# Performance work log

Measured on AMD Instinct MI355X. Metric: run time of the kernel, lower is better.

The kernel has to match this reference:

```python
import jax, jax.numpy as jnp
import numpy as np

D_MODEL = 1024
NUM_HEADS = 16
D_K = D_MODEL // NUM_HEADS
SCALE = float(np.sqrt(D_K))


def setup_inputs() -> dict:
    key = jax.random.key(0)
    ks = jax.random.split(key, 6)
    x = jax.random.normal(ks[0], (2, 2048, D_MODEL), dtype=jnp.float32)
    s = 1.0 / np.sqrt(D_MODEL)
    w_q = jax.random.uniform(ks[1], (D_MODEL, D_MODEL), jnp.float32, -s, s)
    w_k = jax.random.uniform(ks[2], (D_MODEL, D_MODEL), jnp.float32, -s, s)
    w_v = jax.random.uniform(ks[3], (D_MODEL, D_MODEL), jnp.float32, -s, s)
    w_o = jax.random.uniform(ks[4], (D_MODEL, D_MODEL), jnp.float32, -s, s)
    b_o = jax.random.uniform(ks[5], (D_MODEL,), jnp.float32, -s, s)
    return {"x": x, "w_q": w_q, "w_k": w_k, "w_v": w_v, "w_o": w_o, "b_o": b_o}


def reference(x, w_q, w_k, w_v, w_o, b_o):
    B, S, _ = x.shape
    # project and split heads: [B, H, S, d_k]
    def heads(w):
        return (x @ w.T).reshape(B, S, NUM_HEADS, D_K).transpose(0, 2, 1, 3)
    Q, K, V = heads(w_q), heads(w_k), heads(w_v)
    scores = jnp.einsum("bhqd,bhkd->bhqk", Q, K) / SCALE  # [B,H,S,S]
    attn = jax.nn.softmax(scores, axis=-1)
    context = jnp.einsum("bhqk,bhkd->bhqd", attn, V)
    context = context.transpose(0, 2, 1, 3).reshape(B, S, D_MODEL)
    return context @ w_o.T + b_o
```

## Files before the change

### kernel.cpp

```cpp
#include <hip/hip_runtime.h>

typedef unsigned short u16t;
typedef short bf16x8 __attribute__((ext_vector_type(8)));
typedef short bf16x4 __attribute__((ext_vector_type(4)));
typedef float f32x4 __attribute__((ext_vector_type(4)));

#define NHEADS 16
#define SEQ 2048
#define DMODEL 1024
#define HEAD_ELEMS (SEQ * 64)
#define LSTR 72
#define QSTR 40
#define MATE ((size_t)2 * SEQ * DMODEL)
#define CSC 0.1803368801f
#define MB 4.0f

__device__ __forceinline__ u16t f2bf(float f) {
  union { float f; unsigned u; } v; v.f = f;
  unsigned r = v.u + 0x7FFFu + ((v.u >> 16) & 1u);
  return (u16t)(r >> 16);
}
__device__ __forceinline__ float bf2f(u16t b) {
  union { unsigned u; float f; } v; v.u = ((unsigned)b) << 16;
  return v.f;
}
__device__ __forceinline__ float sanef(float x) {
  return fminf(fmaxf(x, -16384.f), 16384.f);
}
__device__ __forceinline__ unsigned pk2(float a, float b) {
  union { float f; unsigned u; } x, y; x.f = a; y.f = b;
  return __builtin_amdgcn_perm(y.u + 0x8000u, x.u + 0x8000u, 0x07060302u);
}
__device__ __forceinline__ bf16x8 cvt8(const float* p) {
  const f32x4* q4 = (const f32x4*)p;
  f32x4 a = q4[0], b = q4[1];
  bf16x8 o;
  o[0] = (short)f2bf(a[0]); o[1] = (short)f2bf(a[1]);
  o[2] = (short)f2bf(a[2]); o[3] = (short)f2bf(a[3]);
  o[4] = (short)f2bf(b[0]); o[5] = (short)f2bf(b[1]);
  o[6] = (short)f2bf(b[2]); o[7] = (short)f2bf(b[3]);
  return o;
}

struct ushort4a { u16t x, y, z, w; } __attribute__((aligned(8)));

__device__ __forceinline__ int detect_bf16_wave(const u16t* p) {
  int lane = threadIdx.x & 63;
  int cnt = 0;
#pragma unroll
  for (int i = 0; i < 8; ++i) {
    int ex = (p[2 * (lane * 8 + i)] >> 7) & 0xFF;
    cnt += (ex >= 100 && ex <= 140) ? 1 : 0;
  }
  cnt += __shfl_xor(cnt, 1);
  cnt += __shfl_xor(cnt, 2);
  cnt += __shfl_xor(cnt, 4);
  cnt += __shfl_xor(cnt, 8);
  cnt += __shfl_xor(cnt, 16);
  cnt += __shfl_xor(cnt, 32);
  return cnt >= 300;
}

__global__ __launch_bounds__(256, 3) void qkv_kernel(
    const void* __restrict__ xv,
    const void* __restrict__ wqv, const void* __restrict__ wkv,
    const void* __restrict__ wvv,
    u16t* __restrict__ q_ws, u16t* __restrict__ k_ws, u16t* __restrict__ vt_ws) {
  __shared__ u16t As[2][128 * QSTR];
  __shared__ u16t Bs[2][128 * QSTR];
  const int bfm = detect_bf16_wave((const u16t*)xv);
  const int tid = threadIdx.x;
  const int bm0 = blockIdx.x * 128;
  const int bn0 = blockIdx.y * 128;
  const int z = blockIdx.z;
  const void* Wv = (z == 0) ? wqv : ((z == 1) ? wkv : wvv);
  const float scale = (z == 0) ? CSC : 1.0f;
  const int lane = tid & 63;
  const int w = tid >> 6;
  const int ln = lane & 15;
  const int quad = lane >> 4;
  const int wm = (w & 1) * 64;
  const int wn = (w >> 1) * 64;

  f32x4 acc[4][4] = {};

  auto do_mfma = [&](int cur) {
    bf16x8 a[4], b[4];
#pragma unroll
    for (int t = 0; t < 4; ++t)
      a[t] = *(const bf16x8*)&As[cur][(wm + t * 16 + ln) * QSTR + quad * 8];
#pragma unroll
    for (int t = 0; t < 4; ++t)
      b[t] = *(const bf16x8*)&Bs[cur][(wn + t * 16 + ln) * QSTR + quad * 8];
    if (z < 2) {
#pragma unroll
      for (int p = 0; p < 4; ++p)
#pragma unroll
        for (int q = 0; q < 4; ++q)
          acc[p][q] = __builtin_amdgcn_mfma_f32_16x16x32_bf16(b[p], a[q], acc[p][q], 0, 0, 0);
    } else {
#pragma unroll
      for (int p = 0; p < 4; ++p)
#pragma unroll
        for (int q = 0; q < 4; ++q)
          acc[p][q] = __builtin_amdgcn_mfma_f32_16x16x32_bf16(a[p], b[q], acc[p][q], 0, 0, 0);
    }
  };

  if (bfm) {
    const u16t* x = (const u16t*)xv;
    const u16t* W = (const u16t*)Wv;
    const int c0 = tid, c1 = tid + 256;
    const int r0 = c0 >> 2, o0 = (c0 & 3) * 8;
    const int r1 = c1 >> 2, o1 = (c1 & 3) * 8;
    const u16t* xa0 = x + (size_t)(bm0 + r0) * DMODEL + o0;
    const u16t* xa1 = x + (size_t)(bm0 + r1) * DMODEL + o1;
    const u16t* wb0 = W + (size_t)(bn0 + r0) * DMODEL + o0;
    const u16t* wb1 = W + (size_t)(bn0 + r1) * DMODEL + o1;
    const int d0 = r0 * QSTR + o0, d1 = r1 * QSTR + o1;

    bf16x8 ra0 = *(const bf16x8*)xa0, ra1 = *(const bf16x8*)xa1;
    bf16x8 rb0 = *(const bf16x8*)wb0, rb1 = *(const bf16x8*)wb1;
    *(bf16x8*)&As[0][d0] = ra0; *(bf16x8*)&As[0][d1] = ra1;
    *(bf16x8*)&Bs[0][d0] = rb0; *(bf16x8*)&Bs[0][d1] = rb1;
    __syncthreads();
    for (int kt = 0; kt < 32; ++kt) {
      int cur = kt & 1;
      if (kt < 31) {
        xa0 += 32; xa1 += 32; wb0 += 32; wb1 += 32;
        ra0 = *(const bf16x8*)xa0; ra1 = *(const bf16x8*)xa1;
        rb0 = *(const bf16x8*)wb0; rb1 = *(const bf16x8*)wb1;
      }
      do_mfma(cur);
      if (kt < 31) {
        int nxt = cur ^ 1;
        *(bf16x8*)&As[nxt][d0] = ra0; *(bf16x8*)&As[nxt][d1] = ra1;
        *(bf16x8*)&Bs[nxt][d0] = rb0; *(bf16x8*)&Bs[nxt][d1] = rb1;
        __syncthreads();
      }
    }
  } else {
    const float* x = (const float*)xv;
    const float* W = (const float*)Wv;
    for (int kt = 0; kt < 32; ++kt) {
      __syncthreads();
#pragma unroll
      for (int j = 0; j < 2; ++j) {
        int c = j * 256 + tid;
        int row = c >> 2, col = (c & 3) * 8;
        *(bf16x8*)&As[0][row * QSTR + col] = cvt8(x + (size_t)(bm0 + row) * DMODEL + kt * 32 + col);
        *(bf16x8*)&Bs[0][row * QSTR + col] = cvt8(W + (size_t)(bn0 + row) * DMODEL + kt * 32 + col);
      }
      __syncthreads();
      do_mfma(0);
    }
  }

  if (z < 2) {
    u16t* dst = (z == 0) ? q_ws : k_ws;
#pragma unroll
    for (int p = 0; p < 4; ++p) {
      int n_base = bn0 + wn + p * 16 + quad * 4;
      int h = n_base >> 6, dkb = n_base & 63;
#pragma unroll
      for (int q = 0; q < 4; ++q) {
        int m = bm0 + wm + q * 16 + ln;
        int bb = m >> 11, sq = m & 2047;
        ushort4a pk;
        pk.x = f2bf(sanef(acc[p][q][0]) * scale);
        pk.y = f2bf(sanef(acc[p][q][1]) * scale);
        pk.z = f2bf(sanef(acc[p][q][2]) * scale);
        pk.w = f2bf(sanef(acc[p][q][3]) * scale);
        *(ushort4a*)&dst[(size_t)(bb * NHEADS + h) * HEAD_ELEMS + sq * 64 + dkb] = pk;
      }
    }
  } else {
#pragma unroll
    for (int p = 0; p < 4; ++p) {
      int m_base = bm0 + wm + p * 16 + quad * 4;
      int bb = m_base >> 11, sq = m_base & 2047;
#pragma unroll
      for (int q = 0; q < 4; ++q) {
        int n = bn0 + wn + q * 16 + ln;
        int h = n >> 6, dk = n & 63;
        ushort4a pk;
        pk.x = f2bf(sanef(acc[p][q][0]));
        pk.y = f2bf(sanef(acc[p][q][1]));
        pk.z = f2bf(sanef(acc[p][q][2]));
        pk.w = f2bf(sanef(acc[p][q][3]));
        *(ushort4a*)&vt_ws[(size_t)(bb * NHEADS + h) * HEAD_ELEMS + (size_t)dk * SEQ + sq] = pk;
      }
    }
  }
}

__global__ __launch_bounds__(512, 4) void attn_kernel(
    const u16t* __restrict__ q_ws, const u16t* __restrict__ k_ws,
    const u16t* __restrict__ vt_ws, u16t* __restrict__ ctx_ws) {
  __shared__ u16t Ks[2][64 * LSTR];
  __shared__ u16t Vt[2][64 * LSTR];
  const int tid = threadIdx.x;
  const int w = tid >> 6;
  const int lane = tid & 63;
  const int ln = lane & 15;
  const int quad = lane >> 4;
  const int bh = blockIdx.y;
  const size_t base = (size_t)bh * HEAD_ELEMS;
  const int q0w = blockIdx.x * 128 + w * 16;

  bf16x8 aq[2];
#pragma unroll
  for (int ks = 0; ks < 2; ++ks)
    aq[ks] = *(const bf16x8*)(q_ws + base + (size_t)(q0w + ln) * 64 + ks * 32 + quad * 8);

  const int r = tid >> 3;
  const int cc = (tid & 7) * 8;
  const int d = r * LSTR + cc;
  const u16t* kp = k_ws + base + (size_t)tid * 8;
  const u16t* vp = vt_ws + base + (size_t)r * SEQ + cc;

  f32x4 accO[4] = {};
  float psum = 0.f;

  bf16x8 rk = *(const bf16x8*)kp;
  bf16x8 rv = *(const bf16x8*)vp;
  *(bf16x8*)&Ks[0][d] = rk;
  *(bf16x8*)&Vt[0][d] = rv;
  __syncthreads();

  for (int kt = 0; kt < 32; ++kt) {
    const int cur = kt & 1;
    if (kt < 31) {
      kp += 4096; vp += 64;
      rk = *(const bf16x8*)kp;
      rv = *(const bf16x8*)vp;
    }

    f32x4 st[4];
#pragma unroll
    for (int nt = 0; nt < 4; ++nt) {
      st[nt][0] = -MB; st[nt][1] = -MB; st[nt][2] = -MB; st[nt][3] = -MB;
    }
#pragma unroll
    for (int nt = 0; nt < 4; ++nt)
#pragma unroll
      for (int ks = 0; ks < 2; ++ks) {
        bf16x8 bk = *(const bf16x8*)&Ks[cur][(nt * 16 + ln) * LSTR + ks * 32 + quad * 8];
        st[nt] = __builtin_amdgcn_mfma_f32_16x16x32_bf16(bk, aq[ks], st[nt], 0, 0, 0);
      }

#pragma unroll
    for (int pp = 0; pp < 2; ++pp) {
      float pv[8];
#pragma unroll
      for (int j = 0; j < 4; ++j) {
        pv[j]     = exp2f(st[2 * pp][j]);
        pv[4 + j] = exp2f(st[2 * pp + 1][j]);
      }
      psum += ((pv[0] + pv[1]) + (pv[2] + pv[3])) + ((pv[4] + pv[5]) + (pv[6] + pv[7]));
      union { unsigned u[4]; bf16x8 v; } ap;
      ap.u[0] = pk2(pv[0], pv[1]);
      ap.u[1] = pk2(pv[2], pv[3]);
      ap.u[2] = pk2(pv[4], pv[5]);
      ap.u[3] = pk2(pv[6], pv[7]);
#pragma unroll
      for (int dt = 0; dt < 4; ++dt) {
        const u16t* vrow = &Vt[cur][(dt * 16 + ln) * LSTR + quad * 4];
        bf16x4 lo = *(const bf16x4*)(vrow + (2 * pp) * 16);
        bf16x4 hi = *(const bf16x4*)(vrow + (2 * pp + 1) * 16);
        bf16x8 bb = __builtin_shufflevector(lo, hi, 0, 1, 2, 3, 4, 5, 6, 7);
        accO[dt] = __builtin_amdgcn_mfma_f32_16x16x32_bf16(ap.v, bb, accO[dt], 0, 0, 0);
      }
    }

    if (kt < 31) {
      const int nxt = cur ^ 1;
      *(bf16x8*)&Ks[nxt][d] = rk;
      *(bf16x8*)&Vt[nxt][d] = rv;
      __syncthreads();
    }
  }

  psum += __shfl_xor(psum, 16);
  psum += __shfl_xor(psum, 32);
  float inv[4];
#pragma unroll
  for (int rr = 0; rr < 4; ++rr) {
    float lq = __shfl(psum, quad * 4 + rr);
    inv[rr] = 1.0f / fmaxf(lq, 1e-20f);
  }
#pragma unroll
  for (int dt = 0; dt < 4; ++dt)
#pragma unroll
    for (int rr = 0; rr < 4; ++rr)
      ctx_ws[base + (size_t)(q0w + quad * 4 + rr) * 64 + dt * 16 + ln] =
          f2bf(accO[dt][rr] * inv[rr]);
}

__global__ __launch_bounds__(256, 4) void outproj_kernel(
    const u16t* __restrict__ ctx, const void* __restrict__ wov,
    const void* __restrict__ bov_, void* __restrict__ outv) {
  __shared__ u16t As[2][64 * LSTR];
  __shared__ u16t Bs[2][64 * LSTR];
  const int bfm = detect_bf16_wave((const u16t*)wov);
  const int tid = threadIdx.x;
  const int bm0 = blockIdx.x * 64;
  const int bn0 = blockIdx.y * 64;
  const int lane = tid & 63;
  const int w = tid >> 6;
  const int ln = lane & 15;
  const int quad = lane >> 4;
  const int wm = (w & 1) * 32;
  const int wn = (w >> 1) * 32;

  f32x4 acc[2][2] = {};

  auto do_mfma = [&](int cur) {
    bf16x8 a[2][2], b[2][2];
#pragma unroll
    for (int t = 0; t < 2; ++t)
#pragma unroll
      for (int ks = 0; ks < 2; ++ks) {
        a[t][ks] = *(const bf16x8*)&As[cur][(wm + t * 16 + ln) * LSTR + ks * 32 + quad * 8];
        b[t][ks] = *(const bf16x8*)&Bs[cur][(wn + t * 16 + ln) * LSTR + ks * 32 + quad * 8];
      }
#pragma unroll
    for (int p = 0; p < 2; ++p)
#pragma unroll
      for (int q = 0; q < 2; ++q)
#pragma unroll
        for (int ks = 0; ks < 2; ++ks)
          acc[p][q] = __builtin_amdgcn_mfma_f32_16x16x32_bf16(b[p][ks], a[q][ks], acc[p][q], 0, 0, 0);
  };

  const int c0 = tid, c1 = tid + 256;
  const int r0 = c0 >> 3, o0 = (c0 & 7) * 8;
  const int r1 = c1 >> 3, o1 = (c1 & 7) * 8;
  const int d0 = r0 * LSTR + o0, d1 = r1 * LSTR + o1;
  const int m0 = bm0 + r0, m1 = bm0 + r1;
  const u16t* ap0 = ctx + (size_t)((m0 >> 11) * NHEADS) * HEAD_ELEMS + (m0 & 2047) * 64 + o0;
  const u16t* ap1 = ctx + (size_t)((m1 >> 11) * NHEADS) * HEAD_ELEMS + (m1 & 2047) * 64 + o1;

  if (bfm) {
    const u16t* wo = (const u16t*)wov;
    const u16t* bp0 = wo + (size_t)(bn0 + r0) * DMODEL + o0;
    const u16t* bp1 = wo + (size_t)(bn0 + r1) * DMODEL + o1;
    bf16x8 ra0 = *(const bf16x8*)ap0, ra1 = *(const bf16x8*)ap1;
    bf16x8 rb0 = *(const bf16x8*)bp0, rb1 = *(const bf16x8*)bp1;
    *(bf16x8*)&As[0][d0] = ra0; *(bf16x8*)&As[0][d1] = ra1;
    *(bf16x8*)&Bs[0][d0] = rb0; *(bf16x8*)&Bs[0][d1] = rb1;
    __syncthreads();
    for (int kt = 0; kt < 16; ++kt) {
      int cur = kt & 1;
      if (kt < 15) {
        ap0 += HEAD_ELEMS; ap1 += HEAD_ELEMS;
        bp0 += 64; bp1 += 64;
        ra0 = *(const bf16x8*)ap0; ra1 = *(const bf16x8*)ap1;
        rb0 = *(const bf16x8*)bp0; rb1 = *(const bf16x8*)bp1;
      }
      do_mfma(cur);
      if (kt < 15) {
        int nxt = cur ^ 1;
        *(bf16x8*)&As[nxt][d0] = ra0; *(bf16x8*)&As[nxt][d1] = ra1;
        *(bf16x8*)&Bs[nxt][d0] = rb0; *(bf16x8*)&Bs[nxt][d1] = rb1;
        __syncthreads();
      }
    }
  } else {
    const float* wo = (const float*)wov;
    for (int kt = 0; kt < 16; ++kt) {
      __syncthreads();
      *(bf16x8*)&As[0][d0] = *(const bf16x8*)(ap0 + (size_t)kt * HEAD_ELEMS);
      *(bf16x8*)&As[0][d1] = *(const bf16x8*)(ap1 + (size_t)kt * HEAD_ELEMS);
      *(bf16x8*)&Bs[0][d0] = cvt8(wo + (size_t)(bn0 + r0) * DMODEL + kt * 64 + o0);
      *(bf16x8*)&Bs[0][d1] = cvt8(wo + (size_t)(bn0 + r1) * DMODEL + kt * 64 + o1);
      __syncthreads();
      do_mfma(0);
    }
  }

#pragma unroll
  for (int p = 0; p < 2; ++p) {
    int n_base = bn0 + wn + p * 16 + quad * 4;
    float bv0, bv1, bv2, bv3;
    if (bfm) {
      ushort4a bb = *(const ushort4a*)&((const u16t*)bov_)[n_base];
      bv0 = bf2f(bb.x); bv1 = bf2f(bb.y); bv2 = bf2f(bb.z); bv3 = bf2f(bb.w);
    } else {
      const float* bf = (const float*)bov_;
      bv0 = bf[n_base]; bv1 = bf[n_base + 1]; bv2 = bf[n_base + 2]; bv3 = bf[n_base + 3];
    }
#pragma unroll
    for (int q = 0; q < 2; ++q) {
      int m = bm0 + wm + q * 16 + ln;
      float v0 = sanef(acc[p][q][0]) + bv0;
      float v1 = sanef(acc[p][q][1]) + bv1;
      float v2 = sanef(acc[p][q][2]) + bv2;
      float v3 = sanef(acc[p][q][3]) + bv3;
      if (bfm) {
        ushort4a pk; pk.x = f2bf(v0); pk.y = f2bf(v1); pk.z = f2bf(v2); pk.w = f2bf(v3);
        *(ushort4a*)&((u16t*)outv)[(size_t)m * DMODEL + n_base] = pk;
      } else {
        f32x4 pk; pk[0] = v0; pk[1] = v1; pk[2] = v2; pk[3] = v3;
        *(f32x4*)&((float*)outv)[(size_t)m * DMODEL + n_base] = pk;
      }
    }
  }
}

extern "C" void kernel_launch(void* const* d_in, const int* in_sizes, int n_in,
                              void* d_out, int out_size, void* d_ws, size_t ws_size,
                              hipStream_t stream) {
  (void)in_sizes; (void)n_in; (void)out_size; (void)ws_size;
  const void* x  = d_in[0];
  const void* wq = d_in[1];
  const void* wk = d_in[2];
  const void* wv = d_in[3];
  const void* wo = d_in[4];
  const void* bo = d_in[5];

  u16t* q_ws  = (u16t*)d_ws;
  u16t* k_ws  = q_ws + MATE;
  u16t* vt_ws = k_ws + MATE;
  u16t* ctx_ws = q_ws;

  dim3 gA(32, 8, 3);
  qkv_kernel<<<gA, 256, 0, stream>>>(x, wq, wk, wv, q_ws, k_ws, vt_ws);

  dim3 gB(16, 32);
  attn_kernel<<<gB, 512, 0, stream>>>(q_ws, k_ws, vt_ws, ctx_ws);

  dim3 gC(64, 16);
  outproj_kernel<<<gC, 256, 0, stream>>>(ctx_ws, wo, bo, d_out);
}
```

Before: 234.7 us.

## Stage QKV tiles via direct global-to-LDS loads and shrink attention blocks

The QKV projection drops its register-staged double-buffered pipeline for a single unpadded LDS buffer. The bf16 input path now fills it with global_load_lds direct-to-LDS copies, while the fp32 path converts as before but into the unpadded layout. Separately, the attention kernel goes from 512 to 256 threads per block, covering 64 queries per block with twice as many blocks, which is meant to improve occupancy and load balance. The trade-offs are lost global/compute overlap and likely LDS bank conflicts in QKV, plus doubled K/V tile loads per query in attention.

Result: slower. 263.1 us (+12.1%).

```diff
diff --git a/kernel.cpp b/kernel.cpp
--- a/kernel.cpp
+++ b/kernel.cpp
@@ -10,7 +10,6 @@
 #define DMODEL 1024
 #define HEAD_ELEMS (SEQ * 64)
 #define LSTR 72
-#define QSTR 40
 #define MATE ((size_t)2 * SEQ * DMODEL)
 #define CSC 0.1803368801f
 #define MB 4.0f
@@ -42,6 +41,12 @@
   return o;
 }
 
+__device__ __forceinline__ void stage16(const u16t* g, u16t* l) {
+  __builtin_amdgcn_global_load_lds(
+      (const __attribute__((address_space(1))) unsigned int*)g,
+      (__attribute__((address_space(3))) unsigned int*)l, 16, 0, 0);
+}
+
 struct ushort4a { u16t x, y, z, w; } __attribute__((aligned(8)));
 
 __device__ __forceinline__ int detect_bf16_wave(const u16t* p) {
@@ -61,13 +66,13 @@
   return cnt >= 300;
 }
 
-__global__ __launch_bounds__(256, 3) void qkv_kernel(
+__global__ __launch_bounds__(256) void qkv_kernel(
     const void* __restrict__ xv,
     const void* __restrict__ wqv, const void* __restrict__ wkv,
     const void* __restrict__ wvv,
     u16t* __restrict__ q_ws, u16t* __restrict__ k_ws, u16t* __restrict__ vt_ws) {
-  __shared__ u16t As[2][128 * QSTR];
-  __shared__ u16t Bs[2][128 * QSTR];
+  __shared__ u16t As[128 * 32];
+  __shared__ u16t Bs[128 * 32];
   const int bfm = detect_bf16_wave((const u16t*)xv);
   const int tid = threadIdx.x;
   const int bm0 = blockIdx.x * 128;
@@ -84,14 +89,39 @@
 
   f32x4 acc[4][4] = {};
 
-  auto do_mfma = [&](int cur) {
+  for (int kt = 0; kt < 32; ++kt) {
+    __syncthreads();
+    if (bfm) {
+      const u16t* x = (const u16t*)xv;
+      const u16t* W = (const u16t*)Wv;
+#pragma unroll
+      for (int j = 0; j < 2; ++j) {
+        int f = j * 256 + tid;
+        int row = f >> 2;
+        int col = (f & 3) * 8;
+        stage16(x + (size_t)(bm0 + row) * DMODEL + kt * 32 + col, &As[f * 8]);
+        stage16(W + (size_t)(bn0 + row) * DMODEL + kt * 32 + col, &Bs[f * 8]);
+      }
+    } else {
+      const float* x = (const float*)xv;
+      const float* W = (const float*)Wv;
+#pragma unroll
+      for (int j = 0; j < 2; ++j) {
+        int f = j * 256 + tid;
+        int row = f >> 2;
+        int col = (f & 3) * 8;
+        *(bf16x8*)&As[f * 8] = cvt8(x + (size_t)(bm0 + row) * DMODEL + kt * 32 + col);
+        *(bf16x8*)&Bs[f * 8] = cvt8(W + (size_t)(bn0 + row) * DMODEL + kt * 32 + col);
+      }
+    }
+    __syncthreads();
     bf16x8 a[4], b[4];
 #pragma unroll
     for (int t = 0; t < 4; ++t)
-      a[t] = *(const bf16x8*)&As[cur][(wm + t * 16 + ln) * QSTR + quad * 8];
+      a[t] = *(const bf16x8*)&As[(wm + t * 16 + ln) * 32 + quad * 8];
 #pragma unroll
     for (int t = 0; t < 4; ++t)
-      b[t] = *(const bf16x8*)&Bs[cur][(wn + t * 16 + ln) * QSTR + quad * 8];
+      b[t] = *(const bf16x8*)&Bs[(wn + t * 16 + ln) * 32 + quad * 8];
     if (z < 2) {
 #pragma unroll
       for (int p = 0; p < 4; ++p)
@@ -104,55 +134,6 @@
 #pragma unroll
         for (int q = 0; q < 4; ++q)
           acc[p][q] = __builtin_amdgcn_mfma_f32_16x16x32_bf16(a[p], b[q], acc[p][q], 0, 0, 0);
-    }
-  };
-
-  if (bfm) {
-    const u16t* x = (const u16t*)xv;
-    const u16t* W = (const u16t*)Wv;
-    const int c0 = tid, c1 = tid + 256;
-    const int r0 = c0 >> 2, o0 = (c0 & 3) * 8;
-    const int r1 = c1 >> 2, o1 = (c1 & 3) * 8;
-    const u16t* xa0 = x + (size_t)(bm0 + r0) * DMODEL + o0;
-    const u16t* xa1 = x + (size_t)(bm0 + r1) * DMODEL + o1;
-    const u16t* wb0 = W + (size_t)(bn0 + r0) * DMODEL + o0;
-    const u16t* wb1 = W + (size_t)(bn0 + r1) * DMODEL + o1;
-    const int d0 = r0 * QSTR + o0, d1 = r1 * QSTR + o1;
-
-    bf16x8 ra0 = *(const bf16x8*)xa0, ra1 = *(const bf16x8*)xa1;
-    bf16x8 rb0 = *(const bf16x8*)wb0, rb1 = *(const bf16x8*)wb1;
-    *(bf16x8*)&As[0][d0] = ra0; *(bf16x8*)&As[0][d1] = ra1;
-    *(bf16x8*)&Bs[0][d0] = rb0; *(bf16x8*)&Bs[0][d1] = rb1;
-    __syncthreads();
-    for (int kt = 0; kt < 32; ++kt) {
-      int cur = kt & 1;
-      if (kt < 31) {
-        xa0 += 32; xa1 += 32; wb0 += 32; wb1 += 32;
-        ra0 = *(const bf16x8*)xa0; ra1 = *(const bf16x8*)xa1;
-        rb0 = *(const bf16x8*)wb0; rb1 = *(const bf16x8*)wb1;
-      }
-      do_mfma(cur);
-      if (kt < 31) {
-        int nxt = cur ^ 1;
-        *(bf16x8*)&As[nxt][d0] = ra0; *(bf16x8*)&As[nxt][d1] = ra1;
-        *(bf16x8*)&Bs[nxt][d0] = rb0; *(bf16x8*)&Bs[nxt][d1] = rb1;
-        __syncthreads();
-      }
-    }
-  } else {
-    const float* x = (const float*)xv;
-    const float* W = (const float*)Wv;
-    for (int kt = 0; kt < 32; ++kt) {
-      __syncthreads();
-#pragma unroll
-      for (int j = 0; j < 2; ++j) {
-        int c = j * 256 + tid;
-        int row = c >> 2, col = (c & 3) * 8;
-        *(bf16x8*)&As[0][row * QSTR + col] = cvt8(x + (size_t)(bm0 + row) * DMODEL + kt * 32 + col);
-        *(bf16x8*)&Bs[0][row * QSTR + col] = cvt8(W + (size_t)(bn0 + row) * DMODEL + kt * 32 + col);
-      }
-      __syncthreads();
-      do_mfma(0);
     }
   }
 
@@ -194,7 +175,7 @@
   }
 }
 
-__global__ __launch_bounds__(512, 4) void attn_kernel(
+__global__ __launch_bounds__(256, 4) void attn_kernel(
     const u16t* __restrict__ q_ws, const u16t* __restrict__ k_ws,
     const u16t* __restrict__ vt_ws, u16t* __restrict__ ctx_ws) {
   __shared__ u16t Ks[2][64 * LSTR];
@@ -206,34 +187,37 @@
   const int quad = lane >> 4;
   const int bh = blockIdx.y;
   const size_t base = (size_t)bh * HEAD_ELEMS;
-  const int q0w = blockIdx.x * 128 + w * 16;
+  const int q0w = blockIdx.x * 64 + w * 16;
 
   bf16x8 aq[2];
 #pragma unroll
   for (int ks = 0; ks < 2; ++ks)
     aq[ks] = *(const bf16x8*)(q_ws + base + (size_t)(q0w + ln) * 64 + ks * 32 + quad * 8);
 
-  const int r = tid >> 3;
-  const int cc = (tid & 7) * 8;
-  const int d = r * LSTR + cc;
-  const u16t* kp = k_ws + base + (size_t)tid * 8;
-  const u16t* vp = vt_ws + base + (size_t)r * SEQ + cc;
+  const int c0 = tid, c1 = tid + 256;
+  const int r0 = c0 >> 3, cc0 = (c0 & 7) * 8;
+  const int r1 = c1 >> 3, cc1 = (c1 & 7) * 8;
+  const int d0 = r0 * LSTR + cc0, d1 = r1 * LSTR + cc1;
+  const u16t* kp0 = k_ws + base + (size_t)c0 * 8;
+  const u16t* kp1 = k_ws + base + (size_t)c1 * 8;
+  const u16t* vp0 = vt_ws + base + (size_t)r0 * SEQ + cc0;
+  const u16t* vp1 = vt_ws + base + (size_t)r1 * SEQ + cc1;
 
   f32x4 accO[4] = {};
   float psum = 0.f;
 
-  bf16x8 rk = *(const bf16x8*)kp;
-  bf16x8 rv = *(const bf16x8*)vp;
-  *(bf16x8*)&Ks[0][d] = rk;
-  *(bf16x8*)&Vt[0][d] = rv;
+  bf16x8 rk0 = *(const bf16x8*)kp0, rk1 = *(const bf16x8*)kp1;
+  bf16x8 rv0 = *(const bf16x8*)vp0, rv1 = *(const bf16x8*)vp1;
+  *(bf16x8*)&Ks[0][d0] = rk0; *(bf16x8*)&Ks[0][d1] = rk1;
+  *(bf16x8*)&Vt[0][d0] = rv0; *(bf16x8*)&Vt[0][d1] = rv1;
   __syncthreads();
 
   for (int kt = 0; kt < 32; ++kt) {
     const int cur = kt & 1;
     if (kt < 31) {
-      kp += 4096; vp += 64;
-      rk = *(const bf16x8*)kp;
-      rv = *(const bf16x8*)vp;
+      kp0 += 4096; kp1 += 4096; vp0 += 64; vp1 += 64;
+      rk0 = *(const bf16x8*)kp0; rk1 = *(const bf16x8*)kp1;
+      rv0 = *(const bf16x8*)vp0; rv1 = *(const bf16x8*)vp1;
     }
 
     f32x4 st[4];
@@ -275,8 +259,8 @@
 
     if (kt < 31) {
       const int nxt = cur ^ 1;
-      *(bf16x8*)&Ks[nxt][d] = rk;
-      *(bf16x8*)&Vt[nxt][d] = rv;
+      *(bf16x8*)&Ks[nxt][d0] = rk0; *(bf16x8*)&Ks[nxt][d1] = rk1;
+      *(bf16x8*)&Vt[nxt][d0] = rv0; *(bf16x8*)&Vt[nxt][d1] = rv1;
       __syncthreads();
     }
   }
@@ -427,8 +411,8 @@
   dim3 gA(32, 8, 3);
   qkv_kernel<<<gA, 256, 0, stream>>>(x, wq, wk, wv, q_ws, k_ws, vt_ws);
 
-  dim3 gB(16, 32);
-  attn_kernel<<<gB, 512, 0, stream>>>(q_ws, k_ws, vt_ws, ctx_ws);
+  dim3 gB(32, 32);
+  attn_kernel<<<gB, 256, 0, stream>>>(q_ws, k_ws, vt_ws, ctx_ws);
 
   dim3 gC(64, 16);
   outproj_kernel<<<gC, 256, 0, stream>>>(ctx_ws, wo, bo, d_out);
```
